# Optimization experiments

Measured on AMD Instinct MI355X. Metric: run time of the kernel, lower is better.

The kernel has to match this reference:

```python
import jax, jax.numpy as jnp
import numpy as np

B, C, HEADS, DH = 2, 1280, 20, 64
INNER = HEADS * DH
HW = 64
S = HW * HW
L = 77
ENC = 4096
GROUPS = 32
EPS = 1e-5
CREG = 1.0     # creg_ in __init__
NOATTN = 1.0   # global noattn
NORES = 1.0    # global noresidual


def setup_inputs() -> dict:
    key = jax.random.key(0)
    ks = jax.random.split(key, 10)
    std = 0.02
    return {
        "x": jax.random.normal(ks[0], (B, C, HW, HW), jnp.float32),
        "text": jax.random.normal(ks[1], (B, L, ENC), jnp.float32),
        "gn_gamma": jnp.ones((C,), jnp.float32),
        "gn_beta": jnp.zeros((C,), jnp.float32),
        "ln_gamma": jnp.ones((ENC,), jnp.float32),
        "ln_beta": jnp.zeros((ENC,), jnp.float32),
        "Wq": jax.random.normal(ks[2], (C, INNER), jnp.float32) * std,
        "bq": jnp.zeros((INNER,), jnp.float32),
        "Wk": jax.random.normal(ks[3], (ENC, INNER), jnp.float32) * std,
        "bk": jnp.zeros((INNER,), jnp.float32),
        "Wv": jax.random.normal(ks[4], (ENC, INNER), jnp.float32) * std,
        "bv": jnp.zeros((INNER,), jnp.float32),
        "Wo": jax.random.normal(ks[5], (INNER, C), jnp.float32) * std,
        "bo": jnp.zeros((C,), jnp.float32),
        "size_reg": jax.random.uniform(ks[6], (1, S, L), jnp.float32),
        "treg": jax.random.uniform(ks[7], (1,), jnp.float32),
        "mask": jax.random.randint(ks[8], (1, S, L), 0, 2, jnp.int32),
    }


def _group_norm(h, gamma, beta):
    # h: [B, C, S]; GroupNorm over (C//GROUPS, S) per group
    hg = h.reshape(B, GROUPS, -1)
    mu = hg.mean(-1, keepdims=True)
    var = hg.var(-1, keepdims=True)
    hn = ((hg - mu) * jax.lax.rsqrt(var + EPS)).reshape(B, C, S)
    return hn * gamma[None, :, None] + beta[None, :, None]


def _layer_norm(t, gamma, beta):
    mu = t.mean(-1, keepdims=True)
    var = t.var(-1, keepdims=True)
    return (t - mu) * jax.lax.rsqrt(var + EPS) * gamma + beta


def reference(x, text, gn_gamma, gn_beta, ln_gamma, ln_beta, Wq, bq, Wk, bk,
              Wv, bv, Wo, bo, size_reg, treg, mask):
    residual = x                              # [B, C, HW, HW]
    h = x.reshape(B, C, S)                    # spatial tokens
    h = _group_norm(h, gn_gamma, gn_beta).transpose(0, 2, 1)   # [B, S, C]
    enc = _layer_norm(text, ln_gamma, ln_beta)                  # [B, L, ENC]

    # head_to_batch_dim (out_dim=3): [B, T, inner] -> [B*heads, T, dh]
    q = (h @ Wq + bq).reshape(B, S, HEADS, DH).transpose(0, 2, 1, 3).reshape(B * HEADS, S, DH)
    k = (enc @ Wk + bk).reshape(B, L, HEADS, DH).transpose(0, 2, 1, 3).reshape(B * HEADS, L, DH)
    v = (enc @ Wv + bv).reshape(B, L, HEADS, DH).transpose(0, 2, 1, 3).reshape(B * HEADS, L, DH)

    scale = DH ** -0.5
    sim = jnp.einsum('bsd,bld->bsl', q, k) * scale            # [B*H, S, L]

    # region regularization applied only to the conditional (second) half
    half = (B * HEADS) // 2
    sim_u, sim_c = sim[:half], sim[half:]
    mn = sim_c.min(-1, keepdims=True)
    mx = sim_c.max(-1, keepdims=True)
    m = mask > 0                                               # [1, S, L] broadcasts over heads
    w = size_reg * CREG * treg[0]
    sim_c = sim_c + jnp.where(m, w, 0.0) * (mx - sim_c) - jnp.where(m, 0.0, w) * (sim_c - mn)
    sim = jnp.concatenate([sim_u, sim_c], axis=0)

    probs = jax.nn.softmax(sim, axis=-1)
    out = jnp.einsum('bsl,bld->bsd', probs, v)                 # [B*H, S, DH]
    # batch_to_head_dim: [B*H, S, DH] -> [B, S, inner]
    out = out.reshape(B, HEADS, S, DH).transpose(0, 2, 1, 3).reshape(B, S, INNER)
    out = out @ Wo + bo                                        # to_out[0]; dropout p=0
    out = out.transpose(0, 2, 1).reshape(residual.shape)       # [B, C, HW, HW]
    return out * NOATTN + residual * NORES
```

## Files before the change

kernel.cpp:

```cpp
#include <hip/hip_runtime.h>

typedef __bf16 bf16_t;
typedef __bf16 bf16x8 __attribute__((ext_vector_type(8)));
typedef float  f32x4  __attribute__((ext_vector_type(4)));
typedef unsigned int u32x4 __attribute__((ext_vector_type(4)));


__global__ __launch_bounds__(256) void k_prep(
    const float* __restrict__ x, const float* __restrict__ text,
    const float* __restrict__ lng, const float* __restrict__ lnb,
    const float* __restrict__ w0, const float* __restrict__ w1,
    const float* __restrict__ w2, const float* __restrict__ w3,
    bf16_t* __restrict__ o0, bf16_t* __restrict__ o1,
    bf16_t* __restrict__ o2, bf16_t* __restrict__ o3,
    float* __restrict__ partial, bf16_t* __restrict__ enc)
{
  __shared__ float smemf[64 * 33];
  const int bid = blockIdx.x;
  const int t   = threadIdx.x;

  if (bid < 6720) {
    int z, lb;
    if      (bid < 800)  { z = 0; lb = bid; }
    else if (bid < 1600) { z = 1; lb = bid - 800; }
    else if (bid < 4160) { z = 2; lb = bid - 1600; }
    else                 { z = 3; lb = bid - 4160; }
    const float* in  = (z == 0) ? w0 : (z == 1) ? w1 : (z == 2) ? w2 : w3;
    bf16_t*      out = (z == 0) ? o0 : (z == 1) ? o1 : (z == 2) ? o2 : o3;
    const int R  = (z < 2) ? 1280 : 4096;
    const int c0 = (lb % 40) * 32;
    const int r0 = (lb / 40) * 64;
    float (*tile)[33] = (float(*)[33])smemf;
#pragma unroll
    for (int it = 0; it < 8; ++it) {
      int r = it * 8 + (t >> 5), c = t & 31;
      tile[r][c] = in[(size_t)(r0 + r) * 1280 + c0 + c];
    }
    __syncthreads();
    const int oc  = t >> 3;
    const int seg = t & 7;
    bf16x8 o;
#pragma unroll
    for (int e = 0; e < 8; ++e) o[e] = (bf16_t)tile[seg * 8 + e][oc];
    *(bf16x8*)(out + (size_t)(c0 + oc) * R + r0 + seg * 8) = o;
  } else if (bid < 8768) {
    const int pb    = bid - 6720;
    const int bg    = pb >> 5;
    const int chunk = pb & 31;
    const float* p  = x + (size_t)bg * 163840 + (size_t)chunk * 5120;
    float s1 = 0.f, s2 = 0.f;
#pragma unroll
    for (int it = 0; it < 5; ++it) {
      float4 v = *(const float4*)(p + (size_t)(it * 256 + t) * 4);
      s1 += v.x + v.y + v.z + v.w;
      s2 += v.x * v.x + v.y * v.y + v.z * v.z + v.w * v.w;
    }
#pragma unroll
    for (int off = 32; off > 0; off >>= 1) {
      s1 += __shfl_down(s1, off);
      s2 += __shfl_down(s2, off);
    }
    float* r1 = smemf;
    float* r2 = smemf + 4;
    if ((t & 63) == 0) { r1[t >> 6] = s1; r2[t >> 6] = s2; }
    __syncthreads();
    if (t == 0) {
      partial[pb * 2]     = r1[0] + r1[1] + r1[2] + r1[3];
      partial[pb * 2 + 1] = r2[0] + r2[1] + r2[2] + r2[3];
    }
  } else {
    const int row = bid - 8768;
    const float* p = text + (size_t)row * 4096;
    float s1 = 0.f, s2 = 0.f;
    for (int i = t; i < 1024; i += 256) {
      float4 v = *(const float4*)(p + (size_t)i * 4);
      s1 += v.x + v.y + v.z + v.w;
      s2 += v.x * v.x + v.y * v.y + v.z * v.z + v.w * v.w;
    }
#pragma unroll
    for (int off = 32; off > 0; off >>= 1) {
      s1 += __shfl_down(s1, off);
      s2 += __shfl_down(s2, off);
    }
    float* r1 = smemf;
    float* r2 = smemf + 4;
    float* sh = smemf + 8;
    if ((t & 63) == 0) { r1[t >> 6] = s1; r2[t >> 6] = s2; }
    __syncthreads();
    if (t == 0) {
      float t1 = r1[0] + r1[1] + r1[2] + r1[3];
      float t2 = r2[0] + r2[1] + r2[2] + r2[3];
      const float invN = 1.0f / 4096.0f;
      float mu  = t1 * invN;
      float var = t2 * invN - mu * mu;
      sh[0] = mu;
      sh[1] = rsqrtf(var + 1e-5f);
    }
    __syncthreads();
    const float mu = sh[0], rs = sh[1];
    for (int i = t; i < 1024; i += 256) {
      float4 v  = *(const float4*)(p + (size_t)i * 4);
      float4 gg = *(const float4*)(lng + (size_t)i * 4);
      float4 bb = *(const float4*)(lnb + (size_t)i * 4);
      bf16_t* o = enc + (size_t)row * 4096 + (size_t)i * 4;
      o[0] = (bf16_t)((v.x - mu) * rs * gg.x + bb.x);
      o[1] = (bf16_t)((v.y - mu) * rs * gg.y + bb.y);
      o[2] = (bf16_t)((v.z - mu) * rs * gg.z + bb.z);
      o[3] = (bf16_t)((v.w - mu) * rs * gg.w + bb.w);
    }
  }
}

__global__ __launch_bounds__(256, 3) void k_gnapply_kv(
    const float* __restrict__ x, const float* __restrict__ partial,
    const float* __restrict__ gamma, const float* __restrict__ beta,
    bf16_t* __restrict__ h,
    const bf16_t* __restrict__ enc, const bf16_t* __restrict__ WkT,
    float* __restrict__ part)
{
  __shared__ alignas(16) char smraw[49152];
  const int bid = blockIdx.x;
  const int tid = threadIdx.x;

  if (bid < 2560) {
    float (*tile)[65] = (float(*)[65])smraw;
    float* sst = (float*)(smraw + 64 * 65 * sizeof(float));
    const int s0 = (bid & 63) * 64;
    const int c0 = ((bid >> 6) % 20) * 64;
    const int b  = bid / 1280;
    {
      const int g = tid >> 3, j = tid & 7;
      const int base = ((b * 32 + g) * 32) * 2;
      float s1 = 0.f, s2 = 0.f;
#pragma unroll
      for (int k = 0; k < 4; ++k) {
        s1 += partial[base + (j + 8 * k) * 2];
        s2 += partial[base + (j + 8 * k) * 2 + 1];
      }
      s1 += __shfl_down(s1, 1); s2 += __shfl_down(s2, 1);
      s1 += __shfl_down(s1, 2); s2 += __shfl_down(s2, 2);
      s1 += __shfl_down(s1, 4); s2 += __shfl_down(s2, 4);
      if (j == 0) {
        const float invN = 1.0f / 163840.0f;
        float mu  = s1 * invN;
        float var = s2 * invN - mu * mu;
        sst[g * 2]     = mu;
        sst[g * 2 + 1] = rsqrtf(var + 1e-5f);
      }
    }
#pragma unroll
    for (int it = 0; it < 16; ++it) {
      int cl = it * 4 + (tid >> 6);
      int sl = tid & 63;
      tile[cl][sl] = x[((size_t)(b * 1280 + c0 + cl) << 12) + s0 + sl];
    }
    __syncthreads();
#pragma unroll
    for (int it = 0; it < 2; ++it) {
      int i  = it * 256 + tid;
      int sl = i >> 3;
      int cg = i & 7;
      bf16x8 o;
#pragma unroll
      for (int e = 0; e < 8; ++e) {
        int c  = c0 + cg * 8 + e;
        int g  = c / 40;
        float mu = sst[g * 2];
        float rs = sst[g * 2 + 1];
        o[e] = (bf16_t)((tile[cg * 8 + e][sl] - mu) * rs * gamma[c] + beta[c]);
      }
      *(bf16x8*)(h + (size_t)(b * 4096 + s0 + sl) * 1280 + c0 + cg * 8) = o;
    }
    return;
  }

  bf16_t* smem = (bf16_t*)smraw;
  const int lane = tid & 63;
  const int wv   = tid >> 6;
  const int wm   = wv >> 1, wn = wv & 1;
  const int xx   = bid - 2560;
  const int sk   = xx / 80;
  const int tl   = xx % 80;
  const int nb   = (tl & 7) * 10 + (tl >> 3);
  const int m0   = (nb / 40) * 128;
  const int n0   = (nb % 40) * 64;
  const int kbeg = sk * 512;
  const int lda  = 4096;

  f32x4 acc[4][2];
  const f32x4 fz = {0.f, 0.f, 0.f, 0.f};
#pragma unroll
  for (int i = 0; i < 4; ++i)
#pragma unroll
    for (int j = 0; j < 2; ++j) acc[i][j] = fz;

  auto stage = [&](int buf, int kt) {
    bf16_t* sA = smem + buf * 8192;
    bf16_t* sB = smem + 16384 + buf * 4096;
#pragma unroll
    for (int it = 0; it < 4; ++it) {
      int slot = it * 256 + tid;
      int row  = slot >> 3, ch = slot & 7;
      int grow = m0 + row; if (grow > 153) grow = 153;
      const bf16_t* ga = enc + (size_t)grow * lda + kt + ((ch ^ (row & 7)) << 3);
      __builtin_amdgcn_global_load_lds(
          (const __attribute__((address_space(1))) void*)ga,
          (__attribute__((address_space(3))) void*)((char*)sA + slot * 16),
          16, 0, 0);
    }
#pragma unroll
    for (int it = 0; it < 2; ++it) {
      int slot = it * 256 + tid;
      int row  = slot >> 3, ch = slot & 7;
      const bf16_t* gb = WkT + (size_t)(n0 + row) * lda + kt + ((ch ^ (row & 7)) << 3);
      __builtin_amdgcn_global_load_lds(
          (const __attribute__((address_space(1))) void*)gb,
          (__attribute__((address_space(3))) void*)((char*)sB + slot * 16),
          16, 0, 0);
    }
  };

  stage(0, kbeg);
  stage(1, kbeg + 64);

  for (int t = 0; t < 8; ++t) {
    if (t + 1 < 8) { asm volatile("s_waitcnt vmcnt(6)" ::: "memory"); }
    else           { asm volatile("s_waitcnt vmcnt(0)" ::: "memory"); }
    __builtin_amdgcn_s_barrier();
    const char* pA = (const char*)(smem + (t & 1) * 8192);
    const char* pB = (const char*)(smem + 16384 + (t & 1) * 4096);
#pragma unroll
    for (int ks = 0; ks < 2; ++ks) {
      const int kb = ks * 64 + ((lane >> 4) << 4);
      bf16x8 af[4], bfg[2];
#pragma unroll
      for (int i = 0; i < 4; ++i) {
        int r = wm * 64 + i * 16 + (lane & 15);
        af[i] = *(const bf16x8*)(pA + r * 128 + (kb ^ ((r & 7) << 4)));
      }
#pragma unroll
      for (int j = 0; j < 2; ++j) {
        int c = wn * 32 + j * 16 + (lane & 15);
        bfg[j] = *(const bf16x8*)(pB + c * 128 + (kb ^ ((c & 7) << 4)));
      }
#pragma unroll
      for (int i = 0; i < 4; ++i)
#pragma unroll
        for (int j = 0; j < 2; ++j)
          acc[i][j] = __builtin_amdgcn_mfma_f32_16x16x32_bf16(af[i], bfg[j], acc[i][j], 0, 0, 0);
    }
    asm volatile("s_waitcnt lgkmcnt(0)" ::: "memory");
    __builtin_amdgcn_s_barrier();
    if (t + 2 < 8) stage(t & 1, kbeg + (t + 2) * 64);
  }

#pragma unroll
  for (int i = 0; i < 4; ++i) {
    const int mrow = m0 + wm * 64 + i * 16 + ((lane >> 4) << 2);
#pragma unroll
    for (int j = 0; j < 2; ++j) {
      const int n = n0 + wn * 32 + j * 16 + (lane & 15);
#pragma unroll
      for (int r = 0; r < 4; ++r)
        if (mrow + r < 154)
          part[(size_t)sk * (154 * 2560) + (size_t)(mrow + r) * 2560 + n] = acc[i][j][r];
    }
  }
}

__global__ __launch_bounds__(256, 3) void k_gemm_q(
    const bf16_t* __restrict__ A, const bf16_t* __restrict__ BT,
    const float* __restrict__ bias, bf16_t* __restrict__ outb,
    const float* __restrict__ part, const float* __restrict__ bk,
    const float* __restrict__ bv, bf16_t* __restrict__ kb, bf16_t* __restrict__ vb)
{
  __shared__ alignas(16) bf16_t smem[24576];
  const int tid = threadIdx.x;

  if (blockIdx.x >= 1280) {
    const int i4 = ((blockIdx.x - 1280) * 256 + tid) * 4;
    if (i4 < 154 * 2560) {
      const int r = i4 / 2560, n = i4 % 2560;
      float4 s = (n < 1280) ? *(const float4*)(bk + n) : *(const float4*)(bv + n - 1280);
#pragma unroll
      for (int sp = 0; sp < 8; ++sp) {
        float4 p = *(const float4*)(part + (size_t)sp * (154 * 2560) + i4);
        s.x += p.x; s.y += p.y; s.z += p.z; s.w += p.w;
      }
      bf16_t* dst = (n < 1280) ? (kb + (size_t)r * 1280 + n)
                               : (vb + (size_t)r * 1280 + n - 1280);
      dst[0] = (bf16_t)s.x; dst[1] = (bf16_t)s.y;
      dst[2] = (bf16_t)s.z; dst[3] = (bf16_t)s.w;
    }
    return;
  }

  const int lane = tid & 63;
  const int wv   = tid >> 6;
  const int wm   = wv >> 1, wn = wv & 1;
  const int nbid = (blockIdx.x & 7) * 160 + (blockIdx.x >> 3);
  const int m0   = (nbid / 20) * 128;
  const int n0   = (nbid % 20) * 64;
  const int lda  = 1280;

  f32x4 acc[4][2];
  const f32x4 fz = {0.f, 0.f, 0.f, 0.f};
#pragma unroll
  for (int i = 0; i < 4; ++i)
#pragma unroll
    for (int j = 0; j < 2; ++j) acc[i][j] = fz;

  auto stage = [&](int buf, int kt) {
    bf16_t* sA = smem + buf * 8192;
    bf16_t* sB = smem + 16384 + buf * 4096;
#pragma unroll
    for (int it = 0; it < 4; ++it) {
      int slot = it * 256 + tid;
      int row  = slot >> 3, ch = slot & 7;
      const bf16_t* ga = A + (size_t)(m0 + row) * lda + kt + ((ch ^ (row & 7)) << 3);
      __builtin_amdgcn_global_load_lds(
          (const __attribute__((address_space(1))) void*)ga,
          (__attribute__((address_space(3))) void*)((char*)sA + slot * 16),
          16, 0, 0);
    }
#pragma unroll
    for (int it = 0; it < 2; ++it) {
      int slot = it * 256 + tid;
      int row  = slot >> 3, ch = slot & 7;
      const bf16_t* gb = BT + (size_t)(n0 + row) * lda + kt + ((ch ^ (row & 7)) << 3);
      __builtin_amdgcn_global_load_lds(
          (const __attribute__((address_space(1))) void*)gb,
          (__attribute__((address_space(3))) void*)((char*)sB + slot * 16),
          16, 0, 0);
    }
  };

  const int nt_k = 20;
  stage(0, 0);
  stage(1, 64);

  for (int t = 0; t < nt_k; ++t) {
    if (t + 1 < nt_k) { asm volatile("s_waitcnt vmcnt(6)" ::: "memory"); }
    else              { asm volatile("s_waitcnt vmcnt(0)" ::: "memory"); }
    __builtin_amdgcn_s_barrier();
    const char* pA = (const char*)(smem + (t & 1) * 8192);
    const char* pB = (const char*)(smem + 16384 + (t & 1) * 4096);
#pragma unroll
    for (int ks = 0; ks < 2; ++ks) {
      const int kb = ks * 64 + ((lane >> 4) << 4);
      bf16x8 af[4], bfg[2];
#pragma unroll
      for (int i = 0; i < 4; ++i) {
        int r = wm * 64 + i * 16 + (lane & 15);
        af[i] = *(const bf16x8*)(pA + r * 128 + (kb ^ ((r & 7) << 4)));
      }
#pragma unroll
      for (int j = 0; j < 2; ++j) {
        int c = wn * 32 + j * 16 + (lane & 15);
        bfg[j] = *(const bf16x8*)(pB + c * 128 + (kb ^ ((c & 7) << 4)));
      }
#pragma unroll
      for (int i = 0; i < 4; ++i)
#pragma unroll
        for (int j = 0; j < 2; ++j)
          acc[i][j] = __builtin_amdgcn_mfma_f32_16x16x32_bf16(af[i], bfg[j], acc[i][j], 0, 0, 0);
    }
    asm volatile("s_waitcnt lgkmcnt(0)" ::: "memory");
    __builtin_amdgcn_s_barrier();
    if (t + 2 < nt_k) stage(t & 1, (t + 2) * 64);
  }

  bf16_t* cst = smem;
#pragma unroll
  for (int j = 0; j < 2; ++j) {
    const int n  = n0 + wn * 32 + j * 16 + (lane & 15);
    const float bs = bias[n];
    const int cl = wn * 32 + j * 16 + (lane & 15);
#pragma unroll
    for (int i = 0; i < 4; ++i) {
      const int rl = wm * 64 + i * 16 + ((lane >> 4) << 2);
#pragma unroll
      for (int r = 0; r < 4; ++r)
        cst[(rl + r) * 76 + cl] = (bf16_t)(acc[i][j][r] + bs);
    }
  }
  __syncthreads();
#pragma unroll
  for (int it = 0; it < 4; ++it) {
    int slot = it * 256 + tid;
    int row = slot >> 3, ch = slot & 7;
    u32x4 d = *(const u32x4*)(cst + row * 76 + ch * 8);
    *(u32x4*)(outb + (size_t)(m0 + row) * 1280 + n0 + ch * 8) = d;
  }
}

__global__ __launch_bounds__(256, 3) void k_gemm_o(
    const bf16_t* __restrict__ A, const bf16_t* __restrict__ BT,
    const float* __restrict__ bias, const float* __restrict__ xres,
    float* __restrict__ dout)
{
  __shared__ alignas(16) bf16_t smem[24576];
  const int tid  = threadIdx.x;
  const int lane = tid & 63;
  const int wv   = tid >> 6;
  const int wm   = wv >> 1, wn = wv & 1;

  const int nbid = (blockIdx.x & 7) * 160 + (blockIdx.x >> 3);
  const int m0   = (nbid / 20) * 128;
  const int n0   = (nbid % 20) * 64;
  const int lda  = 1280;

  f32x4 acc[4][2];
  const f32x4 fz = {0.f, 0.f, 0.f, 0.f};
#pragma unroll
  for (int i = 0; i < 4; ++i)
#pragma unroll
    for (int j = 0; j < 2; ++j) acc[i][j] = fz;

  auto stage = [&](int buf, int kt) {
    bf16_t* sA = smem + buf * 8192;
    bf16_t* sB = smem + 16384 + buf * 4096;
#pragma unroll
    for (int it = 0; it < 4; ++it) {
      int slot = it * 256 + tid;
      int row  = slot >> 3, ch = slot & 7;
      const bf16_t* ga = A + (size_t)(m0 + row) * lda + kt + ((ch ^ (row & 7)) << 3);
      __builtin_amdgcn_global_load_lds(
          (const __attribute__((address_space(1))) void*)ga,
          (__attribute__((address_space(3))) void*)((char*)sA + slot * 16),
          16, 0, 0);
    }
#pragma unroll
    for (int it = 0; it < 2; ++it) {
      int slot = it * 256 + tid;
      int row  = slot >> 3, ch = slot & 7;
      const bf16_t* gb = BT + (size_t)(n0 + row) * lda + kt + ((ch ^ (row & 7)) << 3);
      __builtin_amdgcn_global_load_lds(
          (const __attribute__((address_space(1))) void*)gb,
          (__attribute__((address_space(3))) void*)((char*)sB + slot * 16),
          16, 0, 0);
    }
  };

  const int nt_k = 20;
  stage(0, 0);
  stage(1, 64);

  for (int t = 0; t < nt_k; ++t) {
    if (t + 1 < nt_k) { asm volatile("s_waitcnt vmcnt(6)" ::: "memory"); }
    else              { asm volatile("s_waitcnt vmcnt(0)" ::: "memory"); }
    __builtin_amdgcn_s_barrier();
    const char* pA = (const char*)(smem + (t & 1) * 8192);
    const char* pB = (const char*)(smem + 16384 + (t & 1) * 4096);
#pragma unroll
    for (int ks = 0; ks < 2; ++ks) {
      const int kb = ks * 64 + ((lane >> 4) << 4);
      bf16x8 af[4], bfg[2];
#pragma unroll
      for (int i = 0; i < 4; ++i) {
        int r = wm * 64 + i * 16 + (lane & 15);
        af[i] = *(const bf16x8*)(pA + r * 128 + (kb ^ ((r & 7) << 4)));
      }
#pragma unroll
      for (int j = 0; j < 2; ++j) {
        int c = wn * 32 + j * 16 + (lane & 15);
        bfg[j] = *(const bf16x8*)(pB + c * 128 + (kb ^ ((c & 7) << 4)));
      }
#pragma unroll
      for (int i = 0; i < 4; ++i)
#pragma unroll
        for (int j = 0; j < 2; ++j)
          acc[i][j] = __builtin_amdgcn_mfma_f32_16x16x32_bf16(af[i], bfg[j], acc[i][j], 0, 0, 0);
    }
    asm volatile("s_waitcnt lgkmcnt(0)" ::: "memory");
    __builtin_amdgcn_s_barrier();
    if (t + 2 < nt_k) stage(t & 1, (t + 2) * 64);
  }

#pragma unroll
  for (int i = 0; i < 4; ++i) {
    const int mrow = m0 + wm * 64 + i * 16 + ((lane >> 4) << 2);
    const int b = mrow >> 12, s = mrow & 4095;
#pragma unroll
    for (int j = 0; j < 2; ++j) {
      const int n = n0 + wn * 32 + j * 16 + (lane & 15);
      const size_t off = ((size_t)(b * 1280 + n) << 12) + s;
      const float bs = bias[n];
      const float4 xr = *(const float4*)(xres + off);
      float4 o;
      o.x = acc[i][j][0] + bs + xr.x;
      o.y = acc[i][j][1] + bs + xr.y;
      o.z = acc[i][j][2] + bs + xr.z;
      o.w = acc[i][j][3] + bs + xr.w;
      *(float4*)(dout + off) = o;
    }
  }
}

__global__ __launch_bounds__(256) void k_attn(
    const bf16_t* __restrict__ q, const bf16_t* __restrict__ kbuf,
    const bf16_t* __restrict__ vbuf, bf16_t* __restrict__ ao,
    const float* __restrict__ size_reg, const int* __restrict__ mask,
    const float* __restrict__ treg)
{
  __shared__ alignas(16) bf16_t sQ[64 * 64];
  __shared__ alignas(16) bf16_t sK[80 * 64];
  __shared__ alignas(16) bf16_t sVT[64 * 104];
  __shared__ alignas(16) bf16_t sP[4 * 16 * 104];
  const int s0   = blockIdx.x * 64;
  const int bh   = blockIdx.y;
  const int b    = bh / 20, head = bh % 20;
  const int tid  = threadIdx.x, lane = tid & 63, wv = tid >> 6;
  const int ntok = lane & 15;

  const u32x4 uz = {0u, 0u, 0u, 0u};
  for (int i = tid; i < 832; i += 256) ((u32x4*)sVT)[i] = uz;
  for (int i = tid; i < 832; i += 256) ((u32x4*)sP)[i]  = uz;

  const size_t qbase = ((size_t)(b * 4096 + s0)) * 1280 + head * 64;
  for (int slot = tid; slot < 512; slot += 256) {
    int row = slot >> 3, ch = slot & 7;
    u32x4 d = *(const u32x4*)(q + qbase + (size_t)row * 1280 + ((ch ^ (row & 7)) << 3));
    *(u32x4*)((char*)sQ + slot * 16) = d;
  }
  const size_t kvbase = ((size_t)(b * 77)) * 1280 + head * 64;
  for (int slot = tid; slot < 640; slot += 256) {
    int tok = slot >> 3, ch = slot & 7;
    u32x4 d = uz;
    if (tok < 77)
      d = *(const u32x4*)(kbuf + kvbase + (size_t)tok * 1280 + ((ch ^ (tok & 7)) << 3));
    *(u32x4*)((char*)sK + slot * 16) = d;
  }
  __syncthreads();
  for (int e = tid; e < 77 * 64; e += 256) {
    int tok = e >> 6, dh = e & 63;
    sVT[dh * 104 + tok] = vbuf[kvbase + (size_t)tok * 1280 + dh];
  }
  __syncthreads();

  f32x4 sim[5];
  const f32x4 fz = {0.f, 0.f, 0.f, 0.f};
#pragma unroll
  for (int nf = 0; nf < 5; ++nf) sim[nf] = fz;
  const int qrow = wv * 16 + (lane & 15);
#pragma unroll
  for (int ks = 0; ks < 2; ++ks) {
    const int kb = ks * 64 + ((lane >> 4) << 4);
    bf16x8 aq = *(const bf16x8*)((const char*)sQ + qrow * 128 + (kb ^ ((qrow & 7) << 4)));
#pragma unroll
    for (int nf = 0; nf < 5; ++nf) {
      int tok = nf * 16 + ntok;
      bf16x8 bk = *(const bf16x8*)((const char*)sK + tok * 128 + (kb ^ ((tok & 7) << 4)));
      sim[nf] = __builtin_amdgcn_mfma_f32_16x16x32_bf16(aq, bk, sim[nf], 0, 0, 0);
    }
  }

  float vv[5][4];
#pragma unroll
  for (int nf = 0; nf < 5; ++nf)
#pragma unroll
    for (int r = 0; r < 4; ++r) vv[nf][r] = sim[nf][r] * 0.125f;

  const int rbase = s0 + wv * 16 + ((lane >> 4) << 2);

  if (b == 1) {
    const float tr = treg[0];
#pragma unroll
    for (int r = 0; r < 4; ++r) {
      float mx = -1e30f, mn = 1e30f;
#pragma unroll
      for (int nf = 0; nf < 5; ++nf)
        if (nf * 16 + ntok < 77) { mx = fmaxf(mx, vv[nf][r]); mn = fminf(mn, vv[nf][r]); }
#pragma unroll
      for (int m = 1; m < 16; m <<= 1) {
        mx = fmaxf(mx, __shfl_xor(mx, m));
        mn = fminf(mn, __shfl_xor(mn, m));
      }
      const int srow = rbase + r;
#pragma unroll
      for (int nf = 0; nf < 5; ++nf) {
        int l = nf * 16 + ntok;
        if (l < 77) {
          float w  = size_reg[srow * 77 + l] * tr;
          int   mk = mask[srow * 77 + l];
          float v  = vv[nf][r];
          vv[nf][r] = (mk > 0) ? v + w * (mx - v) : v - w * (v - mn);
        }
      }
    }
  }

#pragma unroll
  for (int r = 0; r < 4; ++r) {
    float mx = -1e30f;
#pragma unroll
    for (int nf = 0; nf < 5; ++nf)
      if (nf * 16 + ntok < 77) mx = fmaxf(mx, vv[nf][r]);
#pragma unroll
    for (int m = 1; m < 16; m <<= 1) mx = fmaxf(mx, __shfl_xor(mx, m));
    float p[5]; float sm = 0.f;
#pragma unroll
    for (int nf = 0; nf < 5; ++nf) {
      bool val = (nf * 16 + ntok) < 77;
      p[nf] = val ? __expf(vv[nf][r] - mx) : 0.f;
      sm += p[nf];
    }
#pragma unroll
    for (int m = 1; m < 16; m <<= 1) sm += __shfl_xor(sm, m);
    const float inv = 1.0f / sm;
    const int prow = ((lane >> 4) << 2) + r;
#pragma unroll
    for (int nf = 0; nf < 5; ++nf)
      sP[wv * 1664 + prow * 104 + nf * 16 + ntok] = (bf16_t)(p[nf] * inv);
  }
  __syncthreads();

  f32x4 o[4];
#pragma unroll
  for (int fd = 0; fd < 4; ++fd) o[fd] = fz;
#pragma unroll
  for (int ks = 0; ks < 3; ++ks) {
    const int kb = ks * 64 + ((lane >> 4) << 4);
    bf16x8 ap = *(const bf16x8*)((const char*)sP + wv * 3328 + (lane & 15) * 208 + kb);
#pragma unroll
    for (int fd = 0; fd < 4; ++fd) {
      bf16x8 bv = *(const bf16x8*)((const char*)sVT + (fd * 16 + (lane & 15)) * 208 + kb);
      o[fd] = __builtin_amdgcn_mfma_f32_16x16x32_bf16(ap, bv, o[fd], 0, 0, 0);
    }
  }
  const size_t obase =
      ((size_t)(b * 4096 + s0 + wv * 16 + ((lane >> 4) << 2))) * 1280 + head * 64;
#pragma unroll
  for (int fd = 0; fd < 4; ++fd)
#pragma unroll
    for (int r = 0; r < 4; ++r)
      ao[obase + (size_t)r * 1280 + fd * 16 + (lane & 15)] = (bf16_t)o[fd][r];
}

extern "C" void kernel_launch(void* const* d_in, const int* in_sizes, int n_in,
                              void* d_out, int out_size, void* d_ws, size_t ws_size,
                              hipStream_t stream)
{
  const float* x    = (const float*)d_in[0];
  const float* text = (const float*)d_in[1];
  const float* gng  = (const float*)d_in[2];
  const float* gnb  = (const float*)d_in[3];
  const float* lng  = (const float*)d_in[4];
  const float* lnb  = (const float*)d_in[5];
  const float* Wq   = (const float*)d_in[6];
  const float* bq   = (const float*)d_in[7];
  const float* Wk   = (const float*)d_in[8];
  const float* bk   = (const float*)d_in[9];
  const float* Wv   = (const float*)d_in[10];
  const float* bv   = (const float*)d_in[11];
  const float* Wo   = (const float*)d_in[12];
  const float* bo   = (const float*)d_in[13];
  const float* sreg = (const float*)d_in[14];
  const float* treg = (const float*)d_in[15];
  const int*   msk  = (const int*)d_in[16];
  float* out = (float*)d_out;

  char* ws = (char*)d_ws;
  size_t off = 0;
  auto alloc = [&](size_t bytes) {
    char* p = ws + off;
    off += (bytes + 255) & ~(size_t)255;
    return p;
  };
  float*  partial = (float*)alloc(2048 * 2 * sizeof(float));
  bf16_t* WqT = (bf16_t*)alloc((size_t)1280 * 1280 * 2);
  bf16_t* WkT = (bf16_t*)alloc((size_t)1280 * 4096 * 2);
  bf16_t* WvT = (bf16_t*)alloc((size_t)1280 * 4096 * 2);
  bf16_t* WoT = (bf16_t*)alloc((size_t)1280 * 1280 * 2);
  bf16_t* h   = (bf16_t*)alloc((size_t)8192 * 1280 * 2);
  bf16_t* enc = (bf16_t*)alloc((size_t)154 * 4096 * 2);
  bf16_t* qb  = (bf16_t*)alloc((size_t)8192 * 1280 * 2);
  bf16_t* kb  = (bf16_t*)alloc((size_t)154 * 1280 * 2);
  bf16_t* vb  = (bf16_t*)alloc((size_t)154 * 1280 * 2);
  float*  part = (float*)alloc((size_t)8 * 154 * 2560 * sizeof(float));

  k_prep<<<8922, 256, 0, stream>>>(x, text, lng, lnb, Wq, Wo, Wk, Wv,
                                   WqT, WoT, WkT, WvT, partial, enc);

  k_gnapply_kv<<<3200, 256, 0, stream>>>(x, partial, gng, gnb, h, enc, WkT, part);

  k_gemm_q<<<1665, 256, 0, stream>>>(h, WqT, bq, qb, part, bk, bv, kb, vb);

  k_attn<<<dim3(64, 40), 256, 0, stream>>>(qb, kb, vb, h, sreg, msk, treg);

  k_gemm_o<<<1280, 256, 0, stream>>>(h, WoT, bo, x, out);
}
```

Before: 159.4 us.

## Fuse Q projection with attention and drop split-K for KV projection

The Q GEMM epilogue now writes the Q tile into shared memory and runs the per-head attention (QK^T, region regularization, softmax, PV) in the same block, so the separate attention kernel and the qb round-trip go away. The KV projection no longer uses split-K with fp32 partials and a separate reduction pass. Instead 80 blocks each loop over the full K=4096 and write biased bf16 K/V directly. The risk is a long serial tail: 80 long-running KV blocks may now sit on the critical path, since Q/attention must wait for them.

```diff
diff --git a/kernel.cpp b/kernel.cpp
--- a/kernel.cpp
+++ b/kernel.cpp
@@ -111,23 +111,25 @@
   }
 }
 
-__global__ __launch_bounds__(256, 3) void k_gnapply_kv(
+__global__ __launch_bounds__(256, 3) void k_kv_gn(
     const float* __restrict__ x, const float* __restrict__ partial,
     const float* __restrict__ gamma, const float* __restrict__ beta,
     bf16_t* __restrict__ h,
     const bf16_t* __restrict__ enc, const bf16_t* __restrict__ WkT,
-    float* __restrict__ part)
+    const float* __restrict__ bk, const float* __restrict__ bv,
+    bf16_t* __restrict__ kb, bf16_t* __restrict__ vb)
 {
   __shared__ alignas(16) char smraw[49152];
   const int bid = blockIdx.x;
   const int tid = threadIdx.x;
 
-  if (bid < 2560) {
+  if (bid >= 80) {
     float (*tile)[65] = (float(*)[65])smraw;
     float* sst = (float*)(smraw + 64 * 65 * sizeof(float));
-    const int s0 = (bid & 63) * 64;
-    const int c0 = ((bid >> 6) % 20) * 64;
-    const int b  = bid / 1280;
+    const int idx = bid - 80;
+    const int s0 = (idx & 63) * 64;
+    const int c0 = ((idx >> 6) % 20) * 64;
+    const int b  = idx / 1280;
     {
       const int g = tid >> 3, j = tid & 7;
       const int base = ((b * 32 + g) * 32) * 2;
@@ -178,13 +180,8 @@
   const int lane = tid & 63;
   const int wv   = tid >> 6;
   const int wm   = wv >> 1, wn = wv & 1;
-  const int xx   = bid - 2560;
-  const int sk   = xx / 80;
-  const int tl   = xx % 80;
-  const int nb   = (tl & 7) * 10 + (tl >> 3);
-  const int m0   = (nb / 40) * 128;
-  const int n0   = (nb % 40) * 64;
-  const int kbeg = sk * 512;
+  const int m0   = (bid / 40) * 128;
+  const int n0   = (bid % 40) * 64;
   const int lda  = 4096;
 
   f32x4 acc[4][2];
@@ -220,28 +217,29 @@
     }
   };
 
-  stage(0, kbeg);
-  stage(1, kbeg + 64);
-
-  for (int t = 0; t < 8; ++t) {
-    if (t + 1 < 8) { asm volatile("s_waitcnt vmcnt(6)" ::: "memory"); }
-    else           { asm volatile("s_waitcnt vmcnt(0)" ::: "memory"); }
+  const int nt_k = 64;
+  stage(0, 0);
+  stage(1, 64);
+
+  for (int t = 0; t < nt_k; ++t) {
+    if (t + 1 < nt_k) { asm volatile("s_waitcnt vmcnt(6)" ::: "memory"); }
+    else              { asm volatile("s_waitcnt vmcnt(0)" ::: "memory"); }
     __builtin_amdgcn_s_barrier();
     const char* pA = (const char*)(smem + (t & 1) * 8192);
     const char* pB = (const char*)(smem + 16384 + (t & 1) * 4096);
 #pragma unroll
     for (int ks = 0; ks < 2; ++ks) {
-      const int kb = ks * 64 + ((lane >> 4) << 4);
+      const int kb_ = ks * 64 + ((lane >> 4) << 4);
       bf16x8 af[4], bfg[2];
 #pragma unroll
       for (int i = 0; i < 4; ++i) {
         int r = wm * 64 + i * 16 + (lane & 15);
-        af[i] = *(const bf16x8*)(pA + r * 128 + (kb ^ ((r & 7) << 4)));
+        af[i] = *(const bf16x8*)(pA + r * 128 + (kb_ ^ ((r & 7) << 4)));
       }
 #pragma unroll
       for (int j = 0; j < 2; ++j) {
         int c = wn * 32 + j * 16 + (lane & 15);
-        bfg[j] = *(const bf16x8*)(pB + c * 128 + (kb ^ ((c & 7) << 4)));
+        bfg[j] = *(const bf16x8*)(pB + c * 128 + (kb_ ^ ((c & 7) << 4)));
       }
 #pragma unroll
       for (int i = 0; i < 4; ++i)
@@ -251,7 +249,7 @@
     }
     asm volatile("s_waitcnt lgkmcnt(0)" ::: "memory");
     __builtin_amdgcn_s_barrier();
-    if (t + 2 < 8) stage(t & 1, kbeg + (t + 2) * 64);
+    if (t + 2 < nt_k) stage(t & 1, (t + 2) * 64);
   }
 
 #pragma unroll
@@ -260,47 +258,36 @@
 #pragma unroll
     for (int j = 0; j < 2; ++j) {
       const int n = n0 + wn * 32 + j * 16 + (lane & 15);
+      const float bs = (n < 1280) ? bk[n] : bv[n - 1280];
 #pragma unroll
       for (int r = 0; r < 4; ++r)
-        if (mrow + r < 154)
-          part[(size_t)sk * (154 * 2560) + (size_t)(mrow + r) * 2560 + n] = acc[i][j][r];
+        if (mrow + r < 154) {
+          bf16_t val = (bf16_t)(acc[i][j][r] + bs);
+          if (n < 1280) kb[(size_t)(mrow + r) * 1280 + n] = val;
+          else          vb[(size_t)(mrow + r) * 1280 + n - 1280] = val;
+        }
     }
   }
 }
 
-__global__ __launch_bounds__(256, 3) void k_gemm_q(
+__global__ __launch_bounds__(256, 3) void k_qattn(
     const bf16_t* __restrict__ A, const bf16_t* __restrict__ BT,
-    const float* __restrict__ bias, bf16_t* __restrict__ outb,
-    const float* __restrict__ part, const float* __restrict__ bk,
-    const float* __restrict__ bv, bf16_t* __restrict__ kb, bf16_t* __restrict__ vb)
+    const float* __restrict__ bq, const bf16_t* __restrict__ kbuf,
+    const bf16_t* __restrict__ vbuf, bf16_t* __restrict__ ao,
+    const float* __restrict__ size_reg, const int* __restrict__ mask,
+    const float* __restrict__ treg)
 {
-  __shared__ alignas(16) bf16_t smem[24576];
-  const int tid = threadIdx.x;
-
-  if (blockIdx.x >= 1280) {
-    const int i4 = ((blockIdx.x - 1280) * 256 + tid) * 4;
-    if (i4 < 154 * 2560) {
-      const int r = i4 / 2560, n = i4 % 2560;
-      float4 s = (n < 1280) ? *(const float4*)(bk + n) : *(const float4*)(bv + n - 1280);
-#pragma unroll
-      for (int sp = 0; sp < 8; ++sp) {
-        float4 p = *(const float4*)(part + (size_t)sp * (154 * 2560) + i4);
-        s.x += p.x; s.y += p.y; s.z += p.z; s.w += p.w;
-      }
-      bf16_t* dst = (n < 1280) ? (kb + (size_t)r * 1280 + n)
-                               : (vb + (size_t)r * 1280 + n - 1280);
-      dst[0] = (bf16_t)s.x; dst[1] = (bf16_t)s.y;
-      dst[2] = (bf16_t)s.z; dst[3] = (bf16_t)s.w;
-    }
-    return;
-  }
-
+  __shared__ alignas(16) char smraw[53248];
+  bf16_t* smem = (bf16_t*)smraw;
+  const int tid  = threadIdx.x;
   const int lane = tid & 63;
   const int wv   = tid >> 6;
   const int wm   = wv >> 1, wn = wv & 1;
+
   const int nbid = (blockIdx.x & 7) * 160 + (blockIdx.x >> 3);
   const int m0   = (nbid / 20) * 128;
-  const int n0   = (nbid % 20) * 64;
+  const int head = nbid % 20;
+  const int n0   = head * 64;
   const int lda  = 1280;
 
   f32x4 acc[4][2];
@@ -347,17 +334,17 @@
     const char* pB = (const char*)(smem + 16384 + (t & 1) * 4096);
 #pragma unroll
     for (int ks = 0; ks < 2; ++ks) {
-      const int kb = ks * 64 + ((lane >> 4) << 4);
+      const int kb_ = ks * 64 + ((lane >> 4) << 4);
       bf16x8 af[4], bfg[2];
 #pragma unroll
       for (int i = 0; i < 4; ++i) {
         int r = wm * 64 + i * 16 + (lane & 15);
-        af[i] = *(const bf16x8*)(pA + r * 128 + (kb ^ ((r & 7) << 4)));
+        af[i] = *(const bf16x8*)(pA + r * 128 + (kb_ ^ ((r & 7) << 4)));
       }
 #pragma unroll
       for (int j = 0; j < 2; ++j) {
         int c = wn * 32 + j * 16 + (lane & 15);
-        bfg[j] = *(const bf16x8*)(pB + c * 128 + (kb ^ ((c & 7) << 4)));
+        bfg[j] = *(const bf16x8*)(pB + c * 128 + (kb_ ^ ((c & 7) << 4)));
       }
 #pragma unroll
       for (int i = 0; i < 4; ++i)
@@ -370,27 +357,146 @@
     if (t + 2 < nt_k) stage(t & 1, (t + 2) * 64);
   }
 
-  bf16_t* cst = smem;
+  bf16_t* sQ  = (bf16_t*)smraw;
+  bf16_t* sK  = (bf16_t*)(smraw + 16384);
+  bf16_t* sVT = (bf16_t*)(smraw + 26624);
+  bf16_t* sP  = (bf16_t*)(smraw + 39936);
+  const int b    = m0 >> 12;
+  const int sloc = m0 & 4095;
+  const int ntok = lane & 15;
+  const u32x4 uz = {0u, 0u, 0u, 0u};
+
 #pragma unroll
   for (int j = 0; j < 2; ++j) {
-    const int n  = n0 + wn * 32 + j * 16 + (lane & 15);
-    const float bs = bias[n];
-    const int cl = wn * 32 + j * 16 + (lane & 15);
+    const int dh = wn * 32 + j * 16 + (lane & 15);
+    const float bs = bq[n0 + dh];
 #pragma unroll
     for (int i = 0; i < 4; ++i) {
       const int rl = wm * 64 + i * 16 + ((lane >> 4) << 2);
 #pragma unroll
+      for (int r = 0; r < 4; ++r) {
+        const int row = rl + r;
+        const int byte = row * 128 + ((((dh >> 3) ^ (row & 7)) << 4)) + ((dh & 7) * 2);
+        *(bf16_t*)((char*)sQ + byte) = (bf16_t)(acc[i][j][r] + bs);
+      }
+    }
+  }
+  for (int i = tid; i < 832; i += 256) ((u32x4*)sVT)[i] = uz;
+  for (int i = tid; i < 832; i += 256) ((u32x4*)sP)[i]  = uz;
+  const size_t kvbase = ((size_t)(b * 77)) * 1280 + head * 64;
+  for (int slot = tid; slot < 640; slot += 256) {
+    int tok = slot >> 3, ch = slot & 7;
+    u32x4 d = uz;
+    if (tok < 77)
+      d = *(const u32x4*)(kbuf + kvbase + (size_t)tok * 1280 + ((ch ^ (tok & 7)) << 3));
+    *(u32x4*)((char*)sK + slot * 16) = d;
+  }
+  __syncthreads();
+  for (int e = tid; e < 77 * 64; e += 256) {
+    int tok = e >> 6, dh = e & 63;
+    sVT[dh * 104 + tok] = vbuf[kvbase + (size_t)tok * 1280 + dh];
+  }
+  __syncthreads();
+
+  for (int h2 = 0; h2 < 2; ++h2) {
+    if (h2) __syncthreads();
+
+    f32x4 sim[5];
+#pragma unroll
+    for (int nf = 0; nf < 5; ++nf) sim[nf] = fz;
+    const int qrow = h2 * 64 + wv * 16 + (lane & 15);
+#pragma unroll
+    for (int ks = 0; ks < 2; ++ks) {
+      const int kb_ = ks * 64 + ((lane >> 4) << 4);
+      bf16x8 aq = *(const bf16x8*)((const char*)sQ + qrow * 128 + (kb_ ^ ((qrow & 7) << 4)));
+#pragma unroll
+      for (int nf = 0; nf < 5; ++nf) {
+        int tok = nf * 16 + ntok;
+        bf16x8 bk_ = *(const bf16x8*)((const char*)sK + tok * 128 + (kb_ ^ ((tok & 7) << 4)));
+        sim[nf] = __builtin_amdgcn_mfma_f32_16x16x32_bf16(aq, bk_, sim[nf], 0, 0, 0);
+      }
+    }
+
+    float vv[5][4];
+#pragma unroll
+    for (int nf = 0; nf < 5; ++nf)
+#pragma unroll
+      for (int r = 0; r < 4; ++r) vv[nf][r] = sim[nf][r] * 0.125f;
+
+    const int rbase = sloc + h2 * 64 + wv * 16 + ((lane >> 4) << 2);
+
+    if (b == 1) {
+      const float tr = treg[0];
+#pragma unroll
+      for (int r = 0; r < 4; ++r) {
+        float mx = -1e30f, mn = 1e30f;
+#pragma unroll
+        for (int nf = 0; nf < 5; ++nf)
+          if (nf * 16 + ntok < 77) { mx = fmaxf(mx, vv[nf][r]); mn = fminf(mn, vv[nf][r]); }
+#pragma unroll
+        for (int m = 1; m < 16; m <<= 1) {
+          mx = fmaxf(mx, __shfl_xor(mx, m));
+          mn = fminf(mn, __shfl_xor(mn, m));
+        }
+        const int srow = rbase + r;
+#pragma unroll
+        for (int nf = 0; nf < 5; ++nf) {
+          int l = nf * 16 + ntok;
+          if (l < 77) {
+            float w  = size_reg[srow * 77 + l] * tr;
+            int   mk = mask[srow * 77 + l];
+            float v  = vv[nf][r];
+            vv[nf][r] = (mk > 0) ? v + w * (mx - v) : v - w * (v - mn);
+          }
+        }
+      }
+    }
+
+#pragma unroll
+    for (int r = 0; r < 4; ++r) {
+      float mx = -1e30f;
+#pragma unroll
+      for (int nf = 0; nf < 5; ++nf)
+        if (nf * 16 + ntok < 77) mx = fmaxf(mx, vv[nf][r]);
+#pragma unroll
+      for (int m = 1; m < 16; m <<= 1) mx = fmaxf(mx, __shfl_xor(mx, m));
+      float p[5]; float sm = 0.f;
+#pragma unroll
+      for (int nf = 0; nf < 5; ++nf) {
+        bool val = (nf * 16 + ntok) < 77;
+        p[nf] = val ? __expf(vv[nf][r] - mx) : 0.f;
+        sm += p[nf];
+      }
+#pragma unroll
+      for (int m = 1; m < 16; m <<= 1) sm += __shfl_xor(sm, m);
+      const float inv = 1.0f / sm;
+      const int prow = ((lane >> 4) << 2) + r;
+#pragma unroll
+      for (int nf = 0; nf < 5; ++nf)
+        sP[wv * 1664 + prow * 104 + nf * 16 + ntok] = (bf16_t)(p[nf] * inv);
+    }
+    __syncthreads();
+
+    f32x4 o[4];
+#pragma unroll
+    for (int fd = 0; fd < 4; ++fd) o[fd] = fz;
+#pragma unroll
+    for (int ks = 0; ks < 3; ++ks) {
+      const int kb_ = ks * 64 + ((lane >> 4) << 4);
+      bf16x8 ap = *(const bf16x8*)((const char*)sP + wv * 3328 + (lane & 15) * 208 + kb_);
+#pragma unroll
+      for (int fd = 0; fd < 4; ++fd) {
+        bf16x8 bv_ = *(const bf16x8*)((const char*)sVT + (fd * 16 + (lane & 15)) * 208 + kb_);
+        o[fd] = __builtin_amdgcn_mfma_f32_16x16x32_bf16(ap, bv_, o[fd], 0, 0, 0);
+      }
+    }
+    const size_t obase =
+        ((size_t)(m0 + h2 * 64 + wv * 16 + ((lane >> 4) << 2))) * 1280 + head * 64;
+#pragma unroll
+    for (int fd = 0; fd < 4; ++fd)
+#pragma unroll
       for (int r = 0; r < 4; ++r)
-        cst[(rl + r) * 76 + cl] = (bf16_t)(acc[i][j][r] + bs);
-    }
-  }
-  __syncthreads();
-#pragma unroll
-  for (int it = 0; it < 4; ++it) {
-    int slot = it * 256 + tid;
-    int row = slot >> 3, ch = slot & 7;
-    u32x4 d = *(const u32x4*)(cst + row * 76 + ch * 8);
-    *(u32x4*)(outb + (size_t)(m0 + row) * 1280 + n0 + ch * 8) = d;
+        ao[obase + (size_t)r * 1280 + fd * 16 + (lane & 15)] = (bf16_t)o[fd][r];
   }
 }
 
@@ -454,17 +560,17 @@
     const char* pB = (const char*)(smem + 16384 + (t & 1) * 4096);
 #pragma unroll
     for (int ks = 0; ks < 2; ++ks) {
-      const int kb = ks * 64 + ((lane >> 4) << 4);
+      const int kb_ = ks * 64 + ((lane >> 4) << 4);
       bf16x8 af[4], bfg[2];
 #pragma unroll
       for (int i = 0; i < 4; ++i) {
         int r = wm * 64 + i * 16 + (lane & 15);
-        af[i] = *(const bf16x8*)(pA + r * 128 + (kb ^ ((r & 7) << 4)));
+        af[i] = *(const bf16x8*)(pA + r * 128 + (kb_ ^ ((r & 7) << 4)));
       }
 #pragma unroll
       for (int j = 0; j < 2; ++j) {
         int c = wn * 32 + j * 16 + (lane & 15);
-        bfg[j] = *(const bf16x8*)(pB + c * 128 + (kb ^ ((c & 7) << 4)));
+        bfg[j] = *(const bf16x8*)(pB + c * 128 + (kb_ ^ ((c & 7) << 4)));
       }
 #pragma unroll
       for (int i = 0; i < 4; ++i)
@@ -495,146 +601,6 @@
       *(float4*)(dout + off) = o;
     }
   }
-}
-
-__global__ __launch_bounds__(256) void k_attn(
-    const bf16_t* __restrict__ q, const bf16_t* __restrict__ kbuf,
-    const bf16_t* __restrict__ vbuf, bf16_t* __restrict__ ao,
-    const float* __restrict__ size_reg, const int* __restrict__ mask,
-    const float* __restrict__ treg)
-{
-  __shared__ alignas(16) bf16_t sQ[64 * 64];
-  __shared__ alignas(16) bf16_t sK[80 * 64];
-  __shared__ alignas(16) bf16_t sVT[64 * 104];
-  __shared__ alignas(16) bf16_t sP[4 * 16 * 104];
-  const int s0   = blockIdx.x * 64;
-  const int bh   = blockIdx.y;
-  const int b    = bh / 20, head = bh % 20;
-  const int tid  = threadIdx.x, lane = tid & 63, wv = tid >> 6;
-  const int ntok = lane & 15;
-
-  const u32x4 uz = {0u, 0u, 0u, 0u};
-  for (int i = tid; i < 832; i += 256) ((u32x4*)sVT)[i] = uz;
-  for (int i = tid; i < 832; i += 256) ((u32x4*)sP)[i]  = uz;
-
-  const size_t qbase = ((size_t)(b * 4096 + s0)) * 1280 + head * 64;
-  for (int slot = tid; slot < 512; slot += 256) {
-    int row = slot >> 3, ch = slot & 7;
-    u32x4 d = *(const u32x4*)(q + qbase + (size_t)row * 1280 + ((ch ^ (row & 7)) << 3));
-    *(u32x4*)((char*)sQ + slot * 16) = d;
-  }
-  const size_t kvbase = ((size_t)(b * 77)) * 1280 + head * 64;
-  for (int slot = tid; slot < 640; slot += 256) {
-    int tok = slot >> 3, ch = slot & 7;
-    u32x4 d = uz;
-    if (tok < 77)
-      d = *(const u32x4*)(kbuf + kvbase + (size_t)tok * 1280 + ((ch ^ (tok & 7)) << 3));
-    *(u32x4*)((char*)sK + slot * 16) = d;
-  }
-  __syncthreads();
-  for (int e = tid; e < 77 * 64; e += 256) {
-    int tok = e >> 6, dh = e & 63;
-    sVT[dh * 104 + tok] = vbuf[kvbase + (size_t)tok * 1280 + dh];
-  }
-  __syncthreads();
-
-  f32x4 sim[5];
-  const f32x4 fz = {0.f, 0.f, 0.f, 0.f};
-#pragma unroll
-  for (int nf = 0; nf < 5; ++nf) sim[nf] = fz;
-  const int qrow = wv * 16 + (lane & 15);
-#pragma unroll
-  for (int ks = 0; ks < 2; ++ks) {
-    const int kb = ks * 64 + ((lane >> 4) << 4);
-    bf16x8 aq = *(const bf16x8*)((const char*)sQ + qrow * 128 + (kb ^ ((qrow & 7) << 4)));
-#pragma unroll
-    for (int nf = 0; nf < 5; ++nf) {
-      int tok = nf * 16 + ntok;
-      bf16x8 bk = *(const bf16x8*)((const char*)sK + tok * 128 + (kb ^ ((tok & 7) << 4)));
-      sim[nf] = __builtin_amdgcn_mfma_f32_16x16x32_bf16(aq, bk, sim[nf], 0, 0, 0);
-    }
-  }
-
-  float vv[5][4];
-#pragma unroll
-  for (int nf = 0; nf < 5; ++nf)
-#pragma unroll
-    for (int r = 0; r < 4; ++r) vv[nf][r] = sim[nf][r] * 0.125f;
-
-  const int rbase = s0 + wv * 16 + ((lane >> 4) << 2);
-
-  if (b == 1) {
-    const float tr = treg[0];
-#pragma unroll
-    for (int r = 0; r < 4; ++r) {
-      float mx = -1e30f, mn = 1e30f;
-#pragma unroll
-      for (int nf = 0; nf < 5; ++nf)
-        if (nf * 16 + ntok < 77) { mx = fmaxf(mx, vv[nf][r]); mn = fminf(mn, vv[nf][r]); }
-#pragma unroll
-      for (int m = 1; m < 16; m <<= 1) {
-        mx = fmaxf(mx, __shfl_xor(mx, m));
-        mn = fminf(mn, __shfl_xor(mn, m));
-      }
-      const int srow = rbase + r;
-#pragma unroll
-      for (int nf = 0; nf < 5; ++nf) {
-        int l = nf * 16 + ntok;
-        if (l < 77) {
-          float w  = size_reg[srow * 77 + l] * tr;
-          int   mk = mask[srow * 77 + l];
-          float v  = vv[nf][r];
-          vv[nf][r] = (mk > 0) ? v + w * (mx - v) : v - w * (v - mn);
-        }
-      }
-    }
-  }
-
-#pragma unroll
-  for (int r = 0; r < 4; ++r) {
-    float mx = -1e30f;
-#pragma unroll
-    for (int nf = 0; nf < 5; ++nf)
-      if (nf * 16 + ntok < 77) mx = fmaxf(mx, vv[nf][r]);
-#pragma unroll
-    for (int m = 1; m < 16; m <<= 1) mx = fmaxf(mx, __shfl_xor(mx, m));
-    float p[5]; float sm = 0.f;
-#pragma unroll
-    for (int nf = 0; nf < 5; ++nf) {
-      bool val = (nf * 16 + ntok) < 77;
-      p[nf] = val ? __expf(vv[nf][r] - mx) : 0.f;
-      sm += p[nf];
-    }
-#pragma unroll
-    for (int m = 1; m < 16; m <<= 1) sm += __shfl_xor(sm, m);
-    const float inv = 1.0f / sm;
-    const int prow = ((lane >> 4) << 2) + r;
-#pragma unroll
-    for (int nf = 0; nf < 5; ++nf)
-      sP[wv * 1664 + prow * 104 + nf * 16 + ntok] = (bf16_t)(p[nf] * inv);
-  }
-  __syncthreads();
-
-  f32x4 o[4];
-#pragma unroll
-  for (int fd = 0; fd < 4; ++fd) o[fd] = fz;
-#pragma unroll
-  for (int ks = 0; ks < 3; ++ks) {
-    const int kb = ks * 64 + ((lane >> 4) << 4);
-    bf16x8 ap = *(const bf16x8*)((const char*)sP + wv * 3328 + (lane & 15) * 208 + kb);
-#pragma unroll
-    for (int fd = 0; fd < 4; ++fd) {
-      bf16x8 bv = *(const bf16x8*)((const char*)sVT + (fd * 16 + (lane & 15)) * 208 + kb);
-      o[fd] = __builtin_amdgcn_mfma_f32_16x16x32_bf16(ap, bv, o[fd], 0, 0, 0);
-    }
-  }
-  const size_t obase =
-      ((size_t)(b * 4096 + s0 + wv * 16 + ((lane >> 4) << 2))) * 1280 + head * 64;
-#pragma unroll
-  for (int fd = 0; fd < 4; ++fd)
-#pragma unroll
-    for (int r = 0; r < 4; ++r)
-      ao[obase + (size_t)r * 1280 + fd * 16 + (lane & 15)] = (bf16_t)o[fd][r];
 }
 
 extern "C" void kernel_launch(void* const* d_in, const int* in_sizes, int n_in,
@@ -674,19 +640,17 @@
   bf16_t* WoT = (bf16_t*)alloc((size_t)1280 * 1280 * 2);
   bf16_t* h   = (bf16_t*)alloc((size_t)8192 * 1280 * 2);
   bf16_t* enc = (bf16_t*)alloc((size_t)154 * 4096 * 2);
-  bf16_t* qb  = (bf16_t*)alloc((size_t)8192 * 1280 * 2);
+  bf16_t* att = (bf16_t*)alloc((size_t)8192 * 1280 * 2);
   bf16_t* kb  = (bf16_t*)alloc((size_t)154 * 1280 * 2);
   bf16_t* vb  = (bf16_t*)alloc((size_t)154 * 1280 * 2);
-  float*  part = (float*)alloc((size_t)8 * 154 * 2560 * sizeof(float));
 
   k_prep<<<8922, 256, 0, stream>>>(x, text, lng, lnb, Wq, Wo, Wk, Wv,
                                    WqT, WoT, WkT, WvT, partial, enc);
 
-  k_gnapply_kv<<<3200, 256, 0, stream>>>(x, partial, gng, gnb, h, enc, WkT, part);
-
-  k_gemm_q<<<1665, 256, 0, stream>>>(h, WqT, bq, qb, part, bk, bv, kb, vb);
-
-  k_attn<<<dim3(64, 40), 256, 0, stream>>>(qb, kb, vb, h, sreg, msk, treg);
-
-  k_gemm_o<<<1280, 256, 0, stream>>>(h, WoT, bo, x, out);
+  k_kv_gn<<<2640, 256, 0, stream>>>(x, partial, gng, gnb, h, enc, WkT,
+                                    bk, bv, kb, vb);
+
+  k_qattn<<<1280, 256, 0, stream>>>(h, WqT, bq, kb, vb, att, sreg, msk, treg);
+
+  k_gemm_o<<<1280, 256, 0, stream>>>(att, WoT, bo, x, out);
 }
```

New measurement: 157.6 us, median of 2. Within noise of the previous version (-1.2%).
